# Performance work log

Measured on AMD Instinct MI355X. Metric: run time of the kernel, lower is better.

The kernel has to match this reference:

```python
import jax, jax.numpy as jnp
import numpy as np

D_IN, D_HID, D_OUT, N_ENT = 512, 128, 512, 262144


def setup_inputs() -> dict:
    key = jax.random.key(0)
    ks = jax.random.split(key, 10)
    s_in = 1.0 / np.sqrt(D_IN)
    s_hid = 1.0 / np.sqrt(D_HID)
    return {
        "class_embedding": jax.random.normal(ks[0], (D_IN,), jnp.float32),
        "entity_embeddings": jax.random.normal(ks[1], (N_ENT, D_IN), jnp.float32),
        "Wq": jax.random.normal(ks[2], (D_HID, D_IN), jnp.float32) * s_in,
        "bq": jax.random.normal(ks[3], (D_HID,), jnp.float32) * s_in,
        "Wk": jax.random.normal(ks[4], (D_HID, D_IN), jnp.float32) * s_in,
        "bk": jax.random.normal(ks[5], (D_HID,), jnp.float32) * s_in,
        "Wv": jax.random.normal(ks[6], (D_HID, D_IN), jnp.float32) * s_in,
        "bv": jax.random.normal(ks[7], (D_HID,), jnp.float32) * s_in,
        "Wo": jax.random.normal(ks[8], (D_OUT, D_HID), jnp.float32) * s_hid,
        "bo": jax.random.normal(ks[9], (D_OUT,), jnp.float32) * s_hid,
        "top_k": 5,
    }


def reference(class_embedding, entity_embeddings, Wq, bq, Wk, bk, Wv, bv, Wo, bo, top_k):
    H = Wq.shape[0]
    q = class_embedding @ Wq.T + bq                 # (H,)
    K = entity_embeddings @ Wk.T + bk               # (N, H)
    V = entity_embeddings @ Wv.T + bv               # (N, H)
    logits = (K @ q) / jnp.sqrt(jnp.asarray(H, q.dtype))  # (N,)
    scores = jax.nn.softmax(logits)                 # softmax over all N entities
    k = min(int(top_k), scores.shape[-1])
    topk_scores, topk_idx = jax.lax.top_k(scores, k)
    # gather top-k value rows and take score-weighted sum over the k entries
    weighted_sum = jnp.sum(V[topk_idx] * topk_scores[:, None], axis=0)  # (H,)
    return weighted_sum @ Wo.T + bo                 # (output_dim,)
```

## Files before the change

### kernel.cpp

```cpp
#include <hip/hip_runtime.h>
#include <math.h>

#define D_IN 512
#define D_HID 128
#define D_OUT 512
#define N_ENT 262144

#define K3_BLOCKS 2048
#define WAVES_PER_BLOCK 4
#define TOTAL_WAVES (K3_BLOCKS * WAVES_PER_BLOCK)
#define ROWS_PER_WAVE (N_ENT / TOTAL_WAVES)

#define KV_OFF   0
#define BM_OFF   512
#define BS_OFF   2560
#define BT5_OFF_F 4608

#define INV_SQRT_H 0.08838834764831845f

typedef float f32x4 __attribute__((ext_vector_type(4)));
typedef unsigned long long u64;

__device__ inline u64 pack_key(float v, int idx) {
    unsigned u = __float_as_uint(v);
    u = (u & 0x80000000u) ? ~u : (u | 0x80000000u);
    return ((u64)u << 32) | (unsigned)(~idx);
}
__device__ inline float unpack_val(u64 k) {
    unsigned o = (unsigned)(k >> 32);
    unsigned u = (o & 0x80000000u) ? (o & 0x7FFFFFFFu) : ~o;
    return __uint_as_float(u);
}
__device__ inline int unpack_idx(u64 k) { return (int)~(unsigned)(k & 0xFFFFFFFFu); }

#define INS5(kk) do { u64 _k = (kk); if (_k > t4) {            \
    if (_k > t0)      { t4=t3;t3=t2;t2=t1;t1=t0;t0=_k; }       \
    else if (_k > t1) { t4=t3;t3=t2;t2=t1;t1=_k; }             \
    else if (_k > t2) { t4=t3;t3=t2;t2=_k; }                   \
    else if (_k > t3) { t4=t3;t3=_k; }                         \
    else              { t4=_k; } } } while (0)

__global__ __launch_bounds__(256) void k_front(const float* __restrict__ c,
        const float* __restrict__ Wq, const float* __restrict__ bq,
        const float* __restrict__ Wk, float* __restrict__ ws) {
    __shared__ float qpart[256];
    __shared__ float qs[D_HID];
    __shared__ float kpart[4][64];
    const int t = threadIdx.x;
    {
        const int h = t >> 1, half = t & 1;
        const f32x4* wq = (const f32x4*)(Wq + (h << 9) + (half << 8));
        const f32x4* cv = (const f32x4*)(c + (half << 8));
        float acc = 0.f;
        #pragma unroll 8
        for (int j = 0; j < 64; ++j) {
            f32x4 a = wq[j], b = cv[j];
            acc += a.x*b.x + a.y*b.y + a.z*b.z + a.w*b.w;
        }
        qpart[t] = acc;
    }
    __syncthreads();
    if (t < D_HID) qs[t] = qpart[2*t] + qpart[2*t+1] + bq[t];
    __syncthreads();
    {
        const int g = t >> 6, d = t & 63;
        const int d0 = blockIdx.x * 64;
        const float* col = Wk + (size_t)(g * 32) * D_IN + d0 + d;
        float acc = 0.f;
        #pragma unroll 8
        for (int h = 0; h < 32; ++h) acc += col[(size_t)h * D_IN] * qs[g*32 + h];
        kpart[g][d] = acc;
    }
    __syncthreads();
    if (t < 64) {
        float kv = kpart[0][t] + kpart[1][t] + kpart[2][t] + kpart[3][t];
        ws[KV_OFF + blockIdx.x*64 + t] = kv * INV_SQRT_H;
    }
}

__global__ __launch_bounds__(256) void k_logits(const float* __restrict__ E,
                                                float* __restrict__ ws) {
    const int t = threadIdx.x;
    const int l = t & 63;
    const int w = t >> 6;
    const int wg = blockIdx.x * WAVES_PER_BLOCK + w;
    const long row0 = (long)wg * ROWS_PER_WAVE;

    const f32x4* kv = (const f32x4*)(ws + KV_OFF);
    const f32x4 k0 = kv[l], k1 = kv[64 + l];

    float m = -INFINITY, s = 0.f;
    u64 t0 = 0, t1 = 0, t2 = 0, t3 = 0, t4 = 0;

    for (int it = 0; it < ROWS_PER_WAVE; it += 2) {
        const f32x4* r0 = (const f32x4*)(E + (row0 + it)     * (long)D_IN);
        const f32x4* r1 = (const f32x4*)(E + (row0 + it + 1) * (long)D_IN);
        f32x4 a0 = __builtin_nontemporal_load(r0 + l);
        f32x4 a1 = __builtin_nontemporal_load(r0 + 64 + l);
        f32x4 b0 = __builtin_nontemporal_load(r1 + l);
        f32x4 b1 = __builtin_nontemporal_load(r1 + 64 + l);
        float d0 = a0.x*k0.x + a0.y*k0.y + a0.z*k0.z + a0.w*k0.w
                 + a1.x*k1.x + a1.y*k1.y + a1.z*k1.z + a1.w*k1.w;
        float d1 = b0.x*k0.x + b0.y*k0.y + b0.z*k0.z + b0.w*k0.w
                 + b1.x*k1.x + b1.y*k1.y + b1.z*k1.z + b1.w*k1.w;
        #pragma unroll
        for (int mm = 32; mm > 0; mm >>= 1) {
            d0 += __shfl_xor(d0, mm, 64);
            d1 += __shfl_xor(d1, mm, 64);
        }
        float nm = fmaxf(m, fmaxf(d0, d1));
        s = s * __expf(m - nm) + __expf(d0 - nm) + __expf(d1 - nm);
        m = nm;
        INS5(pack_key(d0, (int)row0 + it));
        INS5(pack_key(d1, (int)row0 + it + 1));
    }

    __shared__ float sm[WAVES_PER_BLOCK], ss[WAVES_PER_BLOCK];
    __shared__ u64 skey[WAVES_PER_BLOCK][5];
    if (l == 0) {
        sm[w] = m; ss[w] = s;
        skey[w][0]=t0; skey[w][1]=t1; skey[w][2]=t2; skey[w][3]=t3; skey[w][4]=t4;
    }
    __syncthreads();
    if (t == 0) {
        float M = fmaxf(fmaxf(sm[0], sm[1]), fmaxf(sm[2], sm[3]));
        float S = ss[0]*__expf(sm[0]-M) + ss[1]*__expf(sm[1]-M)
                + ss[2]*__expf(sm[2]-M) + ss[3]*__expf(sm[3]-M);
        u64 t0=0,t1=0,t2=0,t3=0,t4=0;
        #pragma unroll
        for (int j = 0; j < WAVES_PER_BLOCK*5; ++j) INS5(skey[j/5][j%5]);
        const int b = blockIdx.x;
        ws[BM_OFF + b] = M;
        ws[BS_OFF + b] = S;
        u64* bt = (u64*)ws + (BT5_OFF_F/2) + (size_t)b * 5;
        bt[0]=t0; bt[1]=t1; bt[2]=t2; bt[3]=t3; bt[4]=t4;
    }
}

__global__ __launch_bounds__(1024) void k_tail(const float* __restrict__ E,
        const float* __restrict__ Wv, const float* __restrict__ bv,
        const float* __restrict__ Wo, const float* __restrict__ bo,
        const float* __restrict__ ws, float* __restrict__ out) {
    __shared__ u64   wc[16][5];
    __shared__ float selv[5];
    __shared__ int   seli[5];
    __shared__ float wn[5];
    __shared__ float zp[16];
    __shared__ float Zsh;
    __shared__ float u_sh[D_IN];
    __shared__ float h_sh[D_HID];
    __shared__ float Wsum;
    const int t = threadIdx.x;
    const int l = t & 63;
    const int w = t >> 6;
    const u64* cand = (const u64*)ws + (BT5_OFF_F/2);

    u64 t0=0,t1=0,t2=0,t3=0,t4=0;
    #pragma unroll
    for (int j = 0; j < 10; ++j) INS5(cand[t + j*1024]);

    {
        int pos = 0;
        u64 g0=0,g1=0,g2=0,g3=0,g4=0;
        #pragma unroll
        for (int r = 0; r < 5; ++r) {
            u64 head = pos==0?t0 : pos==1?t1 : pos==2?t2 : pos==3?t3 : pos==4?t4 : 0ULL;
            u64 wm = head;
            #pragma unroll
            for (int mm = 1; mm < 64; mm <<= 1) {
                u64 o = __shfl_xor(wm, mm, 64);
                wm = (o > wm) ? o : wm;
            }
            if (head == wm && wm != 0ULL) pos++;
            if (r==0) g0=wm; else if (r==1) g1=wm; else if (r==2) g2=wm;
            else if (r==3) g3=wm; else g4=wm;
        }
        if (l == 0) { wc[w][0]=g0; wc[w][1]=g1; wc[w][2]=g2; wc[w][3]=g3; wc[w][4]=g4; }
    }
    __syncthreads();

    if (t < 64) {
        int pos = 0;
        #pragma unroll
        for (int r = 0; r < 5; ++r) {
            u64 head = (t < 16 && pos < 5) ? wc[t][pos] : 0ULL;
            u64 wm = head;
            #pragma unroll
            for (int mm = 1; mm < 64; mm <<= 1) {
                u64 o = __shfl_xor(wm, mm, 64);
                wm = (o > wm) ? o : wm;
            }
            if (head == wm && wm != 0ULL) pos++;
            if (t == 0) { selv[r] = unpack_val(wm); seli[r] = unpack_idx(wm); }
        }
    }
    __syncthreads();

    const float M = selv[0];

    {
        float z = ws[BS_OFF + t]      * __expf(ws[BM_OFF + t]      - M)
                + ws[BS_OFF + t+1024] * __expf(ws[BM_OFF + t+1024] - M);
        #pragma unroll
        for (int mm = 1; mm < 64; mm <<= 1) z += __shfl_xor(z, mm, 64);
        if (l == 0) zp[w] = z;
    }
    __syncthreads();
    if (t == 0) {
        float Z = 0.f;
        #pragma unroll
        for (int j = 0; j < 16; ++j) Z += zp[j];
        Zsh = Z;
    }
    __syncthreads();
    if (t < 5) wn[t] = __expf(selv[t] - M) / Zsh;
    __syncthreads();
    if (t == 0) Wsum = wn[0]+wn[1]+wn[2]+wn[3]+wn[4];

    if (t < D_IN) {
        float acc = 0.f;
        #pragma unroll
        for (int r = 0; r < 5; ++r)
            acc += wn[r] * E[(long)seli[r] * D_IN + t];
        u_sh[t] = acc;
    }
    __syncthreads();

    {
        const f32x4* uv = (const f32x4*)u_sh;
        f32x4 u0 = uv[l], u1 = uv[64 + l];
        #pragma unroll
        for (int rr = 0; rr < 8; ++rr) {
            const int j = w * 8 + rr;
            const f32x4* row = (const f32x4*)(Wv + (size_t)j * D_IN);
            f32x4 a0 = row[l], a1 = row[64 + l];
            float d = a0.x*u0.x + a0.y*u0.y + a0.z*u0.z + a0.w*u0.w
                    + a1.x*u1.x + a1.y*u1.y + a1.z*u1.z + a1.w*u1.w;
            #pragma unroll
            for (int mm = 32; mm > 0; mm >>= 1) d += __shfl_xor(d, mm, 64);
            if (l == 0) h_sh[j] = d + Wsum * bv[j];
        }
    }
    __syncthreads();

    {
        const float2* hv = (const float2*)h_sh;
        float2 hh = hv[l];
        #pragma unroll
        for (int rr = 0; rr < 32; ++rr) {
            const int o = w * 32 + rr;
            const float2* row = (const float2*)(Wo + (size_t)o * D_HID);
            float2 a = row[l];
            float d = a.x*hh.x + a.y*hh.y;
            #pragma unroll
            for (int mm = 32; mm > 0; mm >>= 1) d += __shfl_xor(d, mm, 64);
            if (l == 0) out[o] = d + bo[o];
        }
    }
}

extern "C" void kernel_launch(void* const* d_in, const int* in_sizes, int n_in,
                              void* d_out, int out_size, void* d_ws, size_t ws_size,
                              hipStream_t stream) {
    const float* c  = (const float*)d_in[0];
    const float* E  = (const float*)d_in[1];
    const float* Wq = (const float*)d_in[2];
    const float* bq = (const float*)d_in[3];
    const float* Wk = (const float*)d_in[4];
    const float* Wv = (const float*)d_in[6];
    const float* bv = (const float*)d_in[7];
    const float* Wo = (const float*)d_in[8];
    const float* bo = (const float*)d_in[9];
    float* ws  = (float*)d_ws;
    float* out = (float*)d_out;

    hipLaunchKernelGGL(k_front,  dim3(8),         dim3(256),  0, stream, c, Wq, bq, Wk, ws);
    hipLaunchKernelGGL(k_logits, dim3(K3_BLOCKS), dim3(256),  0, stream, E, ws);
    hipLaunchKernelGGL(k_tail,   dim3(1),         dim3(1024), 0, stream,
                       E, Wv, bv, Wo, bo, ws, out);
}
```

Measured before the change: 135.3 us.

## Fuse top-k/softmax merge into last logits block, parallelize V/O projection

New measurement: 227.7 us. 68.3% more time.

```diff
diff --git a/kernel.cpp b/kernel.cpp
--- a/kernel.cpp
+++ b/kernel.cpp
@@ -11,10 +11,14 @@
 #define TOTAL_WAVES (K3_BLOCKS * WAVES_PER_BLOCK)
 #define ROWS_PER_WAVE (N_ENT / TOTAL_WAVES)
 
-#define KV_OFF   0
-#define BM_OFF   512
-#define BS_OFF   2560
+#define KV_OFF    0
+#define BM_OFF    512
+#define BS_OFF    2560
 #define BT5_OFF_F 4608
+#define CNT_F     25088
+#define WN_OFF    25092
+#define SELI_F    25097
+#define WSUM_OFF  25102
 
 #define INV_SQRT_H 0.08838834764831845f
 
@@ -47,6 +51,7 @@
     __shared__ float qs[D_HID];
     __shared__ float kpart[4][64];
     const int t = threadIdx.x;
+    if (blockIdx.x == 0 && t == 0) ((int*)ws)[CNT_F] = 0;
     {
         const int h = t >> 1, half = t & 1;
         const f32x4* wq = (const f32x4*)(Wq + (h << 9) + (half << 8));
@@ -135,29 +140,25 @@
         u64* bt = (u64*)ws + (BT5_OFF_F/2) + (size_t)b * 5;
         bt[0]=t0; bt[1]=t1; bt[2]=t2; bt[3]=t3; bt[4]=t4;
     }
-}
-
-__global__ __launch_bounds__(1024) void k_tail(const float* __restrict__ E,
-        const float* __restrict__ Wv, const float* __restrict__ bv,
-        const float* __restrict__ Wo, const float* __restrict__ bo,
-        const float* __restrict__ ws, float* __restrict__ out) {
-    __shared__ u64   wc[16][5];
-    __shared__ float selv[5];
-    __shared__ int   seli[5];
-    __shared__ float wn[5];
-    __shared__ float zp[16];
-    __shared__ float Zsh;
-    __shared__ float u_sh[D_IN];
-    __shared__ float h_sh[D_HID];
-    __shared__ float Wsum;
-    const int t = threadIdx.x;
-    const int l = t & 63;
-    const int w = t >> 6;
+
+    __shared__ int s_old;
+    if (t == 0) {
+        __threadfence();
+        s_old = atomicAdd((int*)ws + CNT_F, 1);
+    }
+    __syncthreads();
+    if (s_old != K3_BLOCKS - 1) return;
+    __threadfence();
+
+    __shared__ u64   mwc[WAVES_PER_BLOCK][5];
+    __shared__ float selv_sh[5];
+    __shared__ int   seli_sh[5];
+    __shared__ float zp[WAVES_PER_BLOCK];
     const u64* cand = (const u64*)ws + (BT5_OFF_F/2);
 
-    u64 t0=0,t1=0,t2=0,t3=0,t4=0;
-    #pragma unroll
-    for (int j = 0; j < 10; ++j) INS5(cand[t + j*1024]);
+    t0 = 0; t1 = 0; t2 = 0; t3 = 0; t4 = 0;
+    #pragma unroll 8
+    for (int j = 0; j < 40; ++j) INS5(cand[t + 256*j]);
 
     {
         int pos = 0;
@@ -175,15 +176,15 @@
             if (r==0) g0=wm; else if (r==1) g1=wm; else if (r==2) g2=wm;
             else if (r==3) g3=wm; else g4=wm;
         }
-        if (l == 0) { wc[w][0]=g0; wc[w][1]=g1; wc[w][2]=g2; wc[w][3]=g3; wc[w][4]=g4; }
-    }
-    __syncthreads();
-
-    if (t < 64) {
+        if (l == 0) { mwc[w][0]=g0; mwc[w][1]=g1; mwc[w][2]=g2; mwc[w][3]=g3; mwc[w][4]=g4; }
+    }
+    __syncthreads();
+
+    if (w == 0) {
         int pos = 0;
         #pragma unroll
         for (int r = 0; r < 5; ++r) {
-            u64 head = (t < 16 && pos < 5) ? wc[t][pos] : 0ULL;
+            u64 head = (l < WAVES_PER_BLOCK && pos < 5) ? mwc[l][pos] : 0ULL;
             u64 wm = head;
             #pragma unroll
             for (int mm = 1; mm < 64; mm <<= 1) {
@@ -191,66 +192,88 @@
                 wm = (o > wm) ? o : wm;
             }
             if (head == wm && wm != 0ULL) pos++;
-            if (t == 0) { selv[r] = unpack_val(wm); seli[r] = unpack_idx(wm); }
-        }
-    }
-    __syncthreads();
-
-    const float M = selv[0];
-
-    {
-        float z = ws[BS_OFF + t]      * __expf(ws[BM_OFF + t]      - M)
-                + ws[BS_OFF + t+1024] * __expf(ws[BM_OFF + t+1024] - M);
+            if (l == 0) { selv_sh[r] = unpack_val(wm); seli_sh[r] = unpack_idx(wm); }
+        }
+    }
+    __syncthreads();
+
+    const float M = selv_sh[0];
+
+    {
+        float z = 0.f;
+        #pragma unroll
+        for (int k = 0; k < K3_BLOCKS/256; ++k) {
+            int b = t + 256*k;
+            z += ws[BS_OFF + b] * __expf(ws[BM_OFF + b] - M);
+        }
         #pragma unroll
         for (int mm = 1; mm < 64; mm <<= 1) z += __shfl_xor(z, mm, 64);
         if (l == 0) zp[w] = z;
     }
     __syncthreads();
     if (t == 0) {
-        float Z = 0.f;
-        #pragma unroll
-        for (int j = 0; j < 16; ++j) Z += zp[j];
-        Zsh = Z;
-    }
-    __syncthreads();
-    if (t < 5) wn[t] = __expf(selv[t] - M) / Zsh;
-    __syncthreads();
-    if (t == 0) Wsum = wn[0]+wn[1]+wn[2]+wn[3]+wn[4];
-
-    if (t < D_IN) {
+        float Z = zp[0] + zp[1] + zp[2] + zp[3];
+        float wsum = 0.f;
+        #pragma unroll
+        for (int r = 0; r < 5; ++r) {
+            float wv = __expf(selv_sh[r] - M) / Z;
+            ws[WN_OFF + r] = wv;
+            ((int*)ws)[SELI_F + r] = seli_sh[r];
+            wsum += wv;
+        }
+        ws[WSUM_OFF] = wsum;
+    }
+}
+
+__global__ __launch_bounds__(256) void k_vo(const float* __restrict__ E,
+        const float* __restrict__ Wv, const float* __restrict__ bv,
+        const float* __restrict__ Wo, const float* __restrict__ bo,
+        const float* __restrict__ ws, float* __restrict__ out) {
+    __shared__ float u_sh[D_IN];
+    __shared__ float hp[256];
+    __shared__ float h_sh[D_HID];
+    const int t = threadIdx.x;
+    const int l = t & 63;
+    const int w = t >> 6;
+
+    const float wn0 = ws[WN_OFF+0], wn1 = ws[WN_OFF+1], wn2 = ws[WN_OFF+2],
+                wn3 = ws[WN_OFF+3], wn4 = ws[WN_OFF+4];
+    const float Wsum = ws[WSUM_OFF];
+    const int* seli = (const int*)ws + SELI_F;
+    const long i0 = seli[0], i1 = seli[1], i2 = seli[2], i3 = seli[3], i4 = seli[4];
+
+    #pragma unroll
+    for (int p = 0; p < 2; ++p) {
+        const int d = t + p * 256;
+        u_sh[d] = wn0 * E[i0*D_IN + d] + wn1 * E[i1*D_IN + d] + wn2 * E[i2*D_IN + d]
+                + wn3 * E[i3*D_IN + d] + wn4 * E[i4*D_IN + d];
+    }
+    __syncthreads();
+
+    {
+        const int j = t >> 1, half = t & 1;
+        const f32x4* wrow = (const f32x4*)(Wv + (size_t)j * D_IN + half * 256);
+        const f32x4* uv   = (const f32x4*)(u_sh + half * 256);
         float acc = 0.f;
-        #pragma unroll
-        for (int r = 0; r < 5; ++r)
-            acc += wn[r] * E[(long)seli[r] * D_IN + t];
-        u_sh[t] = acc;
-    }
-    __syncthreads();
-
-    {
-        const f32x4* uv = (const f32x4*)u_sh;
-        f32x4 u0 = uv[l], u1 = uv[64 + l];
-        #pragma unroll
-        for (int rr = 0; rr < 8; ++rr) {
-            const int j = w * 8 + rr;
-            const f32x4* row = (const f32x4*)(Wv + (size_t)j * D_IN);
-            f32x4 a0 = row[l], a1 = row[64 + l];
-            float d = a0.x*u0.x + a0.y*u0.y + a0.z*u0.z + a0.w*u0.w
-                    + a1.x*u1.x + a1.y*u1.y + a1.z*u1.z + a1.w*u1.w;
-            #pragma unroll
-            for (int mm = 32; mm > 0; mm >>= 1) d += __shfl_xor(d, mm, 64);
-            if (l == 0) h_sh[j] = d + Wsum * bv[j];
-        }
-    }
+        #pragma unroll 8
+        for (int k = 0; k < 64; ++k) {
+            f32x4 a = wrow[k], b = uv[k];
+            acc += a.x*b.x + a.y*b.y + a.z*b.z + a.w*b.w;
+        }
+        hp[t] = acc;
+    }
+    __syncthreads();
+    if (t < D_HID) h_sh[t] = hp[2*t] + hp[2*t+1] + Wsum * bv[t];
     __syncthreads();
 
     {
         const float2* hv = (const float2*)h_sh;
-        float2 hh = hv[l];
-        #pragma unroll
-        for (int rr = 0; rr < 32; ++rr) {
-            const int o = w * 32 + rr;
-            const float2* row = (const float2*)(Wo + (size_t)o * D_HID);
-            float2 a = row[l];
+        const float2 hh = hv[l];
+        #pragma unroll
+        for (int rr = 0; rr < 2; ++rr) {
+            const int o = blockIdx.x * 8 + w * 2 + rr;
+            const float2* orow = (const float2*)(Wo + (size_t)o * D_HID);
+            float2 a = orow[l];
             float d = a.x*hh.x + a.y*hh.y;
             #pragma unroll
             for (int mm = 32; mm > 0; mm >>= 1) d += __shfl_xor(d, mm, 64);
@@ -274,8 +297,8 @@
     float* ws  = (float*)d_ws;
     float* out = (float*)d_out;
 
-    hipLaunchKernelGGL(k_front,  dim3(8),         dim3(256),  0, stream, c, Wq, bq, Wk, ws);
-    hipLaunchKernelGGL(k_logits, dim3(K3_BLOCKS), dim3(256),  0, stream, E, ws);
-    hipLaunchKernelGGL(k_tail,   dim3(1),         dim3(1024), 0, stream,
+    hipLaunchKernelGGL(k_front,  dim3(8),         dim3(256), 0, stream, c, Wq, bq, Wk, ws);
+    hipLaunchKernelGGL(k_logits, dim3(K3_BLOCKS), dim3(256), 0, stream, E, ws);
+    hipLaunchKernelGGL(k_vo,     dim3(64),        dim3(256), 0, stream,
                        E, Wv, bv, Wo, bo, ws, out);
 }
```
